# Kernel tuning notes

Measured on AMD Instinct MI355X. Metric: run time of the kernel, lower is better.

## Reference

```python
import jax, jax.numpy as jnp
import numpy as np

N_NODES = 50
VOCAB = 21128
EPS = 1e-8


def _gcn(x, edge_index, W, b):
    # x: [N,128], edge_index: [2,E] (src,dst). PyG GCNConv with self-loops and
    # symmetric normalization: out = D^-1/2 (A+I) D^-1/2 (x W) + b
    N = x.shape[0]
    loops = jnp.arange(N, dtype=edge_index.dtype)
    src = jnp.concatenate([edge_index[0], loops])
    dst = jnp.concatenate([edge_index[1], loops])
    xw = x @ W  # [N,10]
    deg = jax.ops.segment_sum(jnp.ones(src.shape[0], x.dtype), dst, num_segments=N)
    dinv = jnp.where(deg > 0, jax.lax.rsqrt(deg), 0.0)
    norm = dinv[src] * dinv[dst]  # [E+N]
    out = jax.ops.segment_sum(norm[:, None] * xw[src], dst, num_segments=N)
    return out + b


def _mp_match(self_feat, cross_feat, assign_w, w1, b1, w2, b2):
    # cosine similarity along feature dim (torch dim=1), eps-clamped norms
    a = assign_w * self_feat   # [50,10]
    c = assign_w * cross_feat  # [50,10]
    dot = jnp.sum(a * c, axis=1)
    na = jnp.maximum(jnp.linalg.norm(a, axis=1), EPS)
    nc = jnp.maximum(jnp.linalg.norm(c, axis=1), EPS)
    dist = dot / (na * nc)  # [50]
    h = jnp.concatenate([dist[:, None], self_feat], axis=-1)  # [50,11]
    h = jax.nn.relu(h @ w1 + b1) @ w2 + b2  # [50,20]
    return h


def _forward_one(emb_table, conv_w, conv_b, cross_w, attn_coef, assign_w,
                 mp_w1, mp_b1, mp_w2, mp_b2, ffn_w1, ffn_b1, ffn_w2, ffn_b2,
                 u_tok, r_tok, u_edge, r_edge):
    u_emb = emb_table[u_tok]  # [50,128]
    r_emb = emb_table[r_tok]
    u_self = _gcn(u_emb, u_edge, conv_w, conv_b)  # [50,10]
    r_self = _gcn(r_emb, r_edge, conv_w, conv_b)
    u_cross = attn_coef @ (r_emb @ cross_w)  # [50,10]
    r_cross = attn_coef @ (u_emb @ cross_w)
    hu = _mp_match(u_self, u_cross, assign_w, mp_w1, mp_b1, mp_w2, mp_b2)
    hr = _mp_match(r_self, r_cross, assign_w, mp_w1, mp_b1, mp_w2, mp_b2)
    g_u = jnp.max(hu, axis=0)  # [20]
    g_r = jnp.max(hr, axis=0)
    feat = jnp.concatenate([g_u, g_r, g_u * g_r, jnp.abs(g_u - g_r)], axis=-1)  # [80]
    logits = jax.nn.relu(feat @ ffn_w1 + ffn_b1) @ ffn_w2 + ffn_b2  # [1]
    return jax.nn.sigmoid(logits)


def setup_inputs() -> dict:
    key = jax.random.key(0)
    ks = jax.random.split(key, 20)
    B, E, D = 4096, 256, 128
    inp = {
        'utterance_input': jax.random.randint(ks[0], (B, N_NODES), 0, VOCAB, dtype=jnp.int32),
        'response_input': jax.random.randint(ks[1], (B, N_NODES), 0, VOCAB, dtype=jnp.int32),
        'utterance_graph_adj': jax.random.randint(ks[2], (B, 2, E), 0, N_NODES, dtype=jnp.int32),
        'response_graph_adj': jax.random.randint(ks[3], (B, 2, E), 0, N_NODES, dtype=jnp.int32),
        'emb_table': jax.random.normal(ks[4], (VOCAB, D), jnp.float32) * 0.02,
        'conv_w': jax.random.normal(ks[5], (D, 10), jnp.float32) * 0.1,
        'conv_b': jnp.zeros((10,), jnp.float32),
        'cross_w': jax.random.uniform(ks[6], (D, 10), jnp.float32),
        'attn_coef': jax.random.uniform(ks[7], (N_NODES, N_NODES), jnp.float32),
        'assign_w': jax.random.uniform(ks[8], (N_NODES, 10), jnp.float32),
        'mp_w1': jax.random.normal(ks[9], (11, 20), jnp.float32) * 0.3,
        'mp_b1': jnp.zeros((20,), jnp.float32),
        'mp_w2': jax.random.normal(ks[10], (20, 20), jnp.float32) * 0.2,
        'mp_b2': jnp.zeros((20,), jnp.float32),
        'ffn_w1': jax.random.normal(ks[11], (80, 40), jnp.float32) * 0.1,
        'ffn_b1': jnp.zeros((40,), jnp.float32),
        'ffn_w2': jax.random.normal(ks[12], (40, 1), jnp.float32) * 0.1,
        'ffn_b2': jnp.zeros((1,), jnp.float32),
    }
    return inp


def reference(utterance_input, response_input, utterance_graph_adj, response_graph_adj,
              emb_table, conv_w, conv_b, cross_w, attn_coef, assign_w,
              mp_w1, mp_b1, mp_w2, mp_b2, ffn_w1, ffn_b1, ffn_w2, ffn_b2):
    f = jax.vmap(_forward_one,
                 in_axes=(None,) * 14 + (0, 0, 0, 0))
    return f(emb_table, conv_w, conv_b, cross_w, attn_coef, assign_w,
             mp_w1, mp_b1, mp_w2, mp_b2, ffn_w1, ffn_b1, ffn_w2, ffn_b2,
             utterance_input, response_input, utterance_graph_adj, response_graph_adj)  # [B,1]
```

## Files before the change

### kernel.cpp

```cpp
#include <hip/hip_runtime.h>
#include <math.h>

#define NN 50
#define XS 12
#define AWW 13

__global__ __launch_bounds__(256) void precompute_proj(
    const float* __restrict__ emb,
    const float* __restrict__ conv_w,
    const float* __restrict__ cross_w,
    const float* __restrict__ attn,
    float* __restrict__ emb_proj,
    float* __restrict__ attn_t,
    int nrows)
{
    if (blockIdx.x == 0) {
        for (int i = threadIdx.x; i < NN * NN; i += 256) {
            int k = i / NN, r = i % NN;
            attn_t[k * NN + r] = attn[r * NN + k];
        }
    }
    const int lane = threadIdx.x & 63;
    const int w    = threadIdx.x >> 6;
    const int r    = blockIdx.x * 64 + lane;
    if (r >= nrows) return;

    const float* wb = (w < 2) ? conv_w : cross_w;
    const int j0 = (w & 1) * 5;

    float acc[5] = {0.0f, 0.0f, 0.0f, 0.0f, 0.0f};
    const float4* rp = (const float4*)(emb + (size_t)r * 128);
#pragma unroll
    for (int q = 0; q < 32; ++q) {
        float4 v = rp[q];
        const float xs[4] = { v.x, v.y, v.z, v.w };
#pragma unroll
        for (int t = 0; t < 4; ++t) {
            const int k = 4 * q + t;
#pragma unroll
            for (int jj = 0; jj < 5; ++jj)
                acc[jj] += xs[t] * wb[k * 10 + j0 + jj];
        }
    }
    float* op = emb_proj + (size_t)r * 20 + w * 5;
#pragma unroll
    for (int jj = 0; jj < 5; ++jj) op[jj] = acc[jj];
}

__global__ __launch_bounds__(128, 5) void gmn_fused(
    const int* __restrict__ tok_u_all, const int* __restrict__ tok_r_all,
    const int* __restrict__ adj_u_all, const int* __restrict__ adj_r_all,
    const float* __restrict__ emb_proj,
    const float* __restrict__ attn_t,
    const float* __restrict__ conv_b,
    const float* __restrict__ assign_w,
    const float* __restrict__ mp_w1, const float* __restrict__ mp_b1,
    const float* __restrict__ mp_w2, const float* __restrict__ mp_b2,
    const float* __restrict__ ffn_w1, const float* __restrict__ ffn_b1,
    const float* __restrict__ ffn_w2, const float* __restrict__ ffn_b2,
    float* __restrict__ out, int E)
{
    const int b    = blockIdx.x;
    const int tid  = threadIdx.x;
    const int lane = tid & 63;
    const int g    = tid >> 6;

    __shared__ __attribute__((aligned(16))) unsigned s_A[2][NN * AWW];
    __shared__ __attribute__((aligned(16))) float    s_xw[2][52 * XS];
    __shared__ __attribute__((aligned(16))) float    s_ci[2][NN * XS];
    __shared__ __attribute__((aligned(16))) float    s_g2[2][24];

    for (int i = lane; i < NN * AWW; i += 64) s_A[g][i] = 0u;
    for (int i = lane; i < 2 * XS; i += 64) s_xw[g][50 * XS + i] = 0.0f;

    float rx[10];
#pragma unroll
    for (int j = 0; j < 10; ++j) rx[j] = 0.0f;

    if (lane < NN) {
        const int t = (g ? tok_r_all : tok_u_all)[(size_t)b * NN + lane];
        const float4* p = (const float4*)(emb_proj + (size_t)t * 20);
        float4 v0 = p[0], v1 = p[1], v2 = p[2], v3 = p[3], v4 = p[4];
        rx[0] = v0.x; rx[1] = v0.y; rx[2] = v0.z; rx[3] = v0.w;
        rx[4] = v1.x; rx[5] = v1.y; rx[6] = v1.z; rx[7] = v1.w;
        rx[8] = v2.x; rx[9] = v2.y;
        float* ci = &s_ci[g][lane * XS];
        *(float4*)(ci)     = make_float4(v2.z, v2.w, v3.x, v3.y);
        *(float4*)(ci + 4) = make_float4(v3.z, v3.w, v4.x, v4.y);
        *(float2*)(ci + 8) = make_float2(v4.z, v4.w);
    }
    {
        const int* adj = (g ? adj_r_all : adj_u_all) + (size_t)b * 2 * E;
        for (int e = lane; e < E; e += 64) {
            int src = adj[e], dst = adj[E + e];
            atomicAdd(&s_A[g][dst * AWW + (src >> 2)], 1u << ((src & 3) * 8));
        }
    }

    unsigned arow[AWW];
    float di = 0.0f;
    if (lane < NN) {
        unsigned s = 0;
#pragma unroll
        for (int kw = 0; kw < AWW; ++kw) {
            unsigned a = s_A[g][lane * AWW + kw];
            arow[kw] = a;
            s += (a & 0xFFu) + ((a >> 8) & 0xFFu) + ((a >> 16) & 0xFFu) + (a >> 24);
        }
        di = rsqrtf(1.0f + (float)s);
#pragma unroll
        for (int j = 0; j < 10; ++j) rx[j] *= di;
        float* x = &s_xw[g][lane * XS];
        *(float4*)(x)     = make_float4(rx[0], rx[1], rx[2], rx[3]);
        *(float4*)(x + 4) = make_float4(rx[4], rx[5], rx[6], rx[7]);
        *(float2*)(x + 8) = make_float2(rx[8], rx[9]);
    }
    __syncthreads();

    float h2[20];
#pragma unroll
    for (int o = 0; o < 20; ++o) h2[o] = -INFINITY;

    if (lane < NN) {
        const int i = lane;

        float cr[10];
#pragma unroll
        for (int j = 0; j < 10; ++j) cr[j] = 0.0f;
        const float* cio = s_ci[g ^ 1];
#pragma unroll 10
        for (int k = 0; k < NN; ++k) {
            float aik = attn_t[k * NN + i];
            const float* crow = &cio[k * XS];
            float4 c0 = *(const float4*)crow;
            float4 c1 = *(const float4*)(crow + 4);
            float2 c2 = *(const float2*)(crow + 8);
            cr[0] += aik * c0.x; cr[1] += aik * c0.y;
            cr[2] += aik * c0.z; cr[3] += aik * c0.w;
            cr[4] += aik * c1.x; cr[5] += aik * c1.y;
            cr[6] += aik * c1.z; cr[7] += aik * c1.w;
            cr[8] += aik * c2.x; cr[9] += aik * c2.y;
        }

        float acc[10];
#pragma unroll
        for (int j = 0; j < 10; ++j) acc[j] = rx[j];
#pragma unroll
        for (int kw = 0; kw < AWW; ++kw) {
            unsigned a = arow[kw];
            float c0 = (float)(a & 0xFFu);
            float c1 = (float)((a >> 8) & 0xFFu);
            float c2 = (float)((a >> 16) & 0xFFu);
            float c3 = (float)(a >> 24);
            const float* x0 = &s_xw[g][(4 * kw) * XS];
#pragma unroll
            for (int t = 0; t < 4; ++t) {
                const float c = (t == 0) ? c0 : (t == 1) ? c1 : (t == 2) ? c2 : c3;
                const float* xr = x0 + t * XS;
                float4 p0 = *(const float4*)xr;
                float4 p1 = *(const float4*)(xr + 4);
                float2 p2 = *(const float2*)(xr + 8);
                acc[0] += c * p0.x; acc[1] += c * p0.y;
                acc[2] += c * p0.z; acc[3] += c * p0.w;
                acc[4] += c * p1.x; acc[5] += c * p1.y;
                acc[6] += c * p1.z; acc[7] += c * p1.w;
                acc[8] += c * p2.x; acc[9] += c * p2.y;
            }
        }
        float sf[10];
#pragma unroll
        for (int j = 0; j < 10; ++j) sf[j] = di * acc[j] + conv_b[j];

        float dot = 0.0f, na2 = 0.0f, nc2 = 0.0f;
        const float2* awp = (const float2*)(assign_w + i * 10);
#pragma unroll
        for (int q = 0; q < 5; ++q) {
            float2 wv = awp[q];
            float a0 = wv.x * sf[2 * q],     d0 = wv.x * cr[2 * q];
            float a1 = wv.y * sf[2 * q + 1], d1 = wv.y * cr[2 * q + 1];
            dot += a0 * d0 + a1 * d1;
            na2 += a0 * a0 + a1 * a1;
            nc2 += d0 * d0 + d1 * d1;
        }
        float dist = dot / (fmaxf(sqrtf(na2), 1e-8f) * fmaxf(sqrtf(nc2), 1e-8f));

        float h1[20];
#pragma unroll
        for (int o = 0; o < 20; ++o) {
            float t = mp_b1[o] + dist * mp_w1[o];
#pragma unroll
            for (int j = 0; j < 10; ++j) t += sf[j] * mp_w1[(1 + j) * 20 + o];
            h1[o] = fmaxf(t, 0.0f);
        }
#pragma unroll
        for (int o = 0; o < 20; ++o) {
            float t = mp_b2[o];
#pragma unroll
            for (int q = 0; q < 20; ++q) t += h1[q] * mp_w2[q * 20 + o];
            h2[o] = t;
        }
    }

#pragma unroll
    for (int o = 0; o < 20; ++o) {
        float v = h2[o];
        v = fmaxf(v, __shfl_xor(v, 1));
        v = fmaxf(v, __shfl_xor(v, 2));
        v = fmaxf(v, __shfl_xor(v, 4));
        v = fmaxf(v, __shfl_xor(v, 8));
        v = fmaxf(v, __shfl_xor(v, 16));
        v = fmaxf(v, __shfl_xor(v, 32));
        h2[o] = v;
    }
    if (lane == 0) {
        *(float4*)&s_g2[g][0]  = make_float4(h2[0],  h2[1],  h2[2],  h2[3]);
        *(float4*)&s_g2[g][4]  = make_float4(h2[4],  h2[5],  h2[6],  h2[7]);
        *(float4*)&s_g2[g][8]  = make_float4(h2[8],  h2[9],  h2[10], h2[11]);
        *(float4*)&s_g2[g][12] = make_float4(h2[12], h2[13], h2[14], h2[15]);
        *(float4*)&s_g2[g][16] = make_float4(h2[16], h2[17], h2[18], h2[19]);
    }
    __syncthreads();

    if (g == 0) {
        float p = 0.0f;
        if (lane < 40) {
            float acc = ffn_b1[lane];
#pragma unroll
            for (int i = 0; i < 20; ++i) {
                float gu = s_g2[0][i], gr = s_g2[1][i];
                acc += gu * ffn_w1[i * 40 + lane]
                     + gr * ffn_w1[(20 + i) * 40 + lane]
                     + gu * gr * ffn_w1[(40 + i) * 40 + lane]
                     + fabsf(gu - gr) * ffn_w1[(60 + i) * 40 + lane];
            }
            p = fmaxf(acc, 0.0f) * ffn_w2[lane];
        }
        p += __shfl_xor(p, 1);  p += __shfl_xor(p, 2);  p += __shfl_xor(p, 4);
        p += __shfl_xor(p, 8);  p += __shfl_xor(p, 16); p += __shfl_xor(p, 32);
        if (lane == 0)
            out[b] = 1.0f / (1.0f + expf(-(p + ffn_b2[0])));
    }
}

extern "C" void kernel_launch(void* const* d_in, const int* in_sizes, int n_in,
                              void* d_out, int out_size, void* d_ws, size_t ws_size,
                              hipStream_t stream)
{
    const int*   tok_u    = (const int*)d_in[0];
    const int*   tok_r    = (const int*)d_in[1];
    const int*   adj_u    = (const int*)d_in[2];
    const int*   adj_r    = (const int*)d_in[3];
    const float* emb      = (const float*)d_in[4];
    const float* conv_w   = (const float*)d_in[5];
    const float* conv_b   = (const float*)d_in[6];
    const float* cross_w  = (const float*)d_in[7];
    const float* attn     = (const float*)d_in[8];
    const float* assign_w = (const float*)d_in[9];
    const float* mp_w1    = (const float*)d_in[10];
    const float* mp_b1    = (const float*)d_in[11];
    const float* mp_w2    = (const float*)d_in[12];
    const float* mp_b2    = (const float*)d_in[13];
    const float* ffn_w1   = (const float*)d_in[14];
    const float* ffn_b1   = (const float*)d_in[15];
    const float* ffn_w2   = (const float*)d_in[16];
    const float* ffn_b2   = (const float*)d_in[17];

    const int B     = in_sizes[0] / 50;
    const int E     = in_sizes[2] / (2 * B);
    const int nrows = in_sizes[4] / 128;

    float* emb_proj = (float*)d_ws;
    float* attn_t   = emb_proj + (size_t)nrows * 20;

    precompute_proj<<<(nrows + 63) / 64, 256, 0, stream>>>(
        emb, conv_w, cross_w, attn, emb_proj, attn_t, nrows);

    gmn_fused<<<B, 128, 0, stream>>>(
        tok_u, tok_r, adj_u, adj_r, emb_proj, attn_t, conv_b,
        assign_w, mp_w1, mp_b1, mp_w2, mp_b2,
        ffn_w1, ffn_b1, ffn_w2, ffn_b2,
        (float*)d_out, E);
}
```

Before: 183.9 us.

## Alias cross and xw shared buffers to cut LDS and raise occupancy

Merges the two per-group shared buffers (cross-input features and normalized xw) into one. The cross-attention product is now computed before the buffer is overwritten, with an extra block barrier separating the phases. The padded last rows are dropped by peeling the final adjacency word to two columns, and launch bounds are raised from 5 to 8 blocks per CU. This lowers LDS use and register budget to allow more resident blocks, at the cost of an extra __syncthreads and possible register spills.

```diff
diff --git a/kernel.cpp b/kernel.cpp
--- a/kernel.cpp
+++ b/kernel.cpp
@@ -47,7 +47,7 @@
     for (int jj = 0; jj < 5; ++jj) op[jj] = acc[jj];
 }
 
-__global__ __launch_bounds__(128, 5) void gmn_fused(
+__global__ __launch_bounds__(128, 8) void gmn_fused(
     const int* __restrict__ tok_u_all, const int* __restrict__ tok_r_all,
     const int* __restrict__ adj_u_all, const int* __restrict__ adj_r_all,
     const float* __restrict__ emb_proj,
@@ -66,12 +66,10 @@
     const int g    = tid >> 6;
 
     __shared__ __attribute__((aligned(16))) unsigned s_A[2][NN * AWW];
-    __shared__ __attribute__((aligned(16))) float    s_xw[2][52 * XS];
-    __shared__ __attribute__((aligned(16))) float    s_ci[2][NN * XS];
+    __shared__ __attribute__((aligned(16))) float    s_buf[2][NN * XS];
     __shared__ __attribute__((aligned(16))) float    s_g2[2][24];
 
     for (int i = lane; i < NN * AWW; i += 64) s_A[g][i] = 0u;
-    for (int i = lane; i < 2 * XS; i += 64) s_xw[g][50 * XS + i] = 0.0f;
 
     float rx[10];
 #pragma unroll
@@ -84,7 +82,7 @@
         rx[0] = v0.x; rx[1] = v0.y; rx[2] = v0.z; rx[3] = v0.w;
         rx[4] = v1.x; rx[5] = v1.y; rx[6] = v1.z; rx[7] = v1.w;
         rx[8] = v2.x; rx[9] = v2.y;
-        float* ci = &s_ci[g][lane * XS];
+        float* ci = &s_buf[g][lane * XS];
         *(float4*)(ci)     = make_float4(v2.z, v2.w, v3.x, v3.y);
         *(float4*)(ci + 4) = make_float4(v3.z, v3.w, v4.x, v4.y);
         *(float2*)(ci + 8) = make_float2(v4.z, v4.w);
@@ -96,9 +94,14 @@
             atomicAdd(&s_A[g][dst * AWW + (src >> 2)], 1u << ((src & 3) * 8));
         }
     }
+    __syncthreads();
 
     unsigned arow[AWW];
     float di = 0.0f;
+    float cr[10];
+#pragma unroll
+    for (int j = 0; j < 10; ++j) cr[j] = 0.0f;
+
     if (lane < NN) {
         unsigned s = 0;
 #pragma unroll
@@ -110,24 +113,9 @@
         di = rsqrtf(1.0f + (float)s);
 #pragma unroll
         for (int j = 0; j < 10; ++j) rx[j] *= di;
-        float* x = &s_xw[g][lane * XS];
-        *(float4*)(x)     = make_float4(rx[0], rx[1], rx[2], rx[3]);
-        *(float4*)(x + 4) = make_float4(rx[4], rx[5], rx[6], rx[7]);
-        *(float2*)(x + 8) = make_float2(rx[8], rx[9]);
-    }
-    __syncthreads();
-
-    float h2[20];
-#pragma unroll
-    for (int o = 0; o < 20; ++o) h2[o] = -INFINITY;
-
-    if (lane < NN) {
+
         const int i = lane;
-
-        float cr[10];
-#pragma unroll
-        for (int j = 0; j < 10; ++j) cr[j] = 0.0f;
-        const float* cio = s_ci[g ^ 1];
+        const float* cio = s_buf[g ^ 1];
 #pragma unroll 10
         for (int k = 0; k < NN; ++k) {
             float aik = attn_t[k * NN + i];
@@ -141,21 +129,54 @@
             cr[6] += aik * c1.z; cr[7] += aik * c1.w;
             cr[8] += aik * c2.x; cr[9] += aik * c2.y;
         }
+    }
+    __syncthreads();
+
+    if (lane < NN) {
+        float* x = &s_buf[g][lane * XS];
+        *(float4*)(x)     = make_float4(rx[0], rx[1], rx[2], rx[3]);
+        *(float4*)(x + 4) = make_float4(rx[4], rx[5], rx[6], rx[7]);
+        *(float2*)(x + 8) = make_float2(rx[8], rx[9]);
+    }
+    __builtin_amdgcn_wave_barrier();
+
+    float h2[20];
+#pragma unroll
+    for (int o = 0; o < 20; ++o) h2[o] = -INFINITY;
+
+    if (lane < NN) {
+        const int i = lane;
 
         float acc[10];
 #pragma unroll
         for (int j = 0; j < 10; ++j) acc[j] = rx[j];
 #pragma unroll
-        for (int kw = 0; kw < AWW; ++kw) {
+        for (int kw = 0; kw < 12; ++kw) {
             unsigned a = arow[kw];
-            float c0 = (float)(a & 0xFFu);
-            float c1 = (float)((a >> 8) & 0xFFu);
-            float c2 = (float)((a >> 16) & 0xFFu);
-            float c3 = (float)(a >> 24);
-            const float* x0 = &s_xw[g][(4 * kw) * XS];
+            float cc[4] = { (float)(a & 0xFFu), (float)((a >> 8) & 0xFFu),
+                            (float)((a >> 16) & 0xFFu), (float)(a >> 24) };
+            const float* x0 = &s_buf[g][(4 * kw) * XS];
 #pragma unroll
             for (int t = 0; t < 4; ++t) {
-                const float c = (t == 0) ? c0 : (t == 1) ? c1 : (t == 2) ? c2 : c3;
+                const float c = cc[t];
+                const float* xr = x0 + t * XS;
+                float4 p0 = *(const float4*)xr;
+                float4 p1 = *(const float4*)(xr + 4);
+                float2 p2 = *(const float2*)(xr + 8);
+                acc[0] += c * p0.x; acc[1] += c * p0.y;
+                acc[2] += c * p0.z; acc[3] += c * p0.w;
+                acc[4] += c * p1.x; acc[5] += c * p1.y;
+                acc[6] += c * p1.z; acc[7] += c * p1.w;
+                acc[8] += c * p2.x; acc[9] += c * p2.y;
+            }
+        }
+        {
+            unsigned a = arow[12];
+            float cc[2] = { (float)(a & 0xFFu), (float)((a >> 8) & 0xFFu) };
+            const float* x0 = &s_buf[g][48 * XS];
+#pragma unroll
+            for (int t = 0; t < 2; ++t) {
+                const float c = cc[t];
                 const float* xr = x0 + t * XS;
                 float4 p0 = *(const float4*)xr;
                 float4 p1 = *(const float4*)(xr + 4);
```

Result: slower. 197.0 us (+7.1%).
